# Performance work log

Hardware: AMD Instinct MI355X
Metric: run time of the kernel (lower is better)

Reference implementation:

```python
import jax, jax.numpy as jnp
import numpy as np

NHLOG2PI = -0.5 * np.log(2.0 * np.pi)


def _log_bessel_i(nu, x):
    # log I_nu(x) via the uniform asymptotic expansion (A&S 9.7.7), accurate for large nu.
    # Replaces the original mpmath besseli loop with a device-friendly closed form.
    z = x / nu
    sq = jnp.sqrt(1.0 + z * z)
    eta = sq + jnp.log(z) - jnp.log1p(sq)
    t = 1.0 / sq
    u1 = (3.0 * t - 5.0 * t ** 3) / 24.0  # first correction term
    return nu * eta - 0.5 * jnp.log(2.0 * jnp.pi * nu) - 0.25 * jnp.log1p(z * z) + jnp.log1p(u1 / nu)


def _log_vmf_partition(d, kappa):
    # log C_d(kappa) = d*(-0.5 log 2pi) + s*log(kappa) - log I_s(kappa), s = d/2 - 1
    s = 0.5 * d - 1.0
    return d * NHLOG2PI + s * jnp.log(kappa) - _log_bessel_i(s, kappa)


def reference(id_samples, kappa_weight, prototypes, targets, project_dim):
    eps_n = 1e-12  # torch F.normalize eps
    eps_c = 1e-8   # torch cosine_similarity eps
    # --- sequential normalized EMA scatter-update of prototypes (faithful to per-sample loop) ---
    norm_samples = id_samples / jnp.maximum(
        jnp.linalg.norm(id_samples, axis=-1, keepdims=True), eps_n)

    def step(protos, inp):
        s_n, t = inp
        new = 0.05 * s_n + 0.95 * protos[t]
        new = new / jnp.maximum(jnp.linalg.norm(new), eps_n)
        return protos.at[t].set(new), None

    protos, _ = jax.lax.scan(step, prototypes, (norm_samples, targets))
    protos = jax.lax.stop_gradient(protos)  # original uses .data.detach()

    # --- cosine similarity [N, C] without materializing the repeated tensors ---
    x_n = id_samples / jnp.maximum(jnp.linalg.norm(id_samples, axis=-1, keepdims=True), eps_c)
    p_n = protos / jnp.maximum(jnp.linalg.norm(protos, axis=-1, keepdims=True), eps_c)
    cos = x_n @ p_n.T  # [N, C]

    kap = jax.nn.relu(kappa_weight)  # [C]
    logits = cos * kap[None, :]
    weight_before_exp = jnp.exp(_log_vmf_partition(float(project_dim), kap))[None, :]  # [1, C]

    # --- weighted vMF NLL ---
    num = weight_before_exp * jnp.exp(logits)
    pred = num / num.sum(-1, keepdims=True)
    p_t = jnp.take_along_axis(pred, targets[:, None], axis=1)[:, 0]
    return -jnp.mean(jnp.log(p_t + 1e-6))


def setup_inputs() -> dict:
    key = jax.random.key(0)
    k1, k2, k3 = jax.random.split(key, 3)
    N, C, D = 16384, 2048, 32
    return {
        "id_samples": jax.random.normal(k1, (N, D), dtype=jnp.float32),
        "kappa_weight": jax.random.uniform(k2, (C,), dtype=jnp.float32),
        "prototypes": jnp.zeros((C, D), dtype=jnp.float32),
        "targets": jax.random.randint(k3, (N,), 0, C),
        "project_dim": D,
    }
```

## Files before the change

kernel.cpp:

```cpp
#include <hip/hip_runtime.h>
#include <hip/hip_bf16.h>
#include <math.h>

#define D 32
#define CAP 28
#define CPB 4
#define SBT 512
#define SSM 16

typedef __attribute__((ext_vector_type(8))) short short8v;
typedef __attribute__((ext_vector_type(4))) float float4v;

static __device__ __forceinline__ unsigned short f2bf(float f) {
    union { __hip_bfloat16 h; unsigned short u; } cv;
    cv.h = __float2bfloat16(f);
    return cv.u;
}
static __device__ __forceinline__ float bf2f(unsigned short u) {
    union { float f; unsigned int i; } c;
    c.i = ((unsigned int)u) << 16;
    return c.f;
}
static __device__ __forceinline__ short8v cvt8(float4 u0, float4 u1) {
    short8v o;
    o[0] = (short)f2bf(u0.x); o[1] = (short)f2bf(u0.y);
    o[2] = (short)f2bf(u0.z); o[3] = (short)f2bf(u0.w);
    o[4] = (short)f2bf(u1.x); o[5] = (short)f2bf(u1.y);
    o[6] = (short)f2bf(u1.z); o[7] = (short)f2bf(u1.w);
    return o;
}

__global__ void k_bucket(const int* __restrict__ tgt, int* __restrict__ cnt,
                         int* __restrict__ list2d, int N) {
    int i = blockIdx.x * blockDim.x + threadIdx.x;
    if (i < N) {
        int t = tgt[i];
        int pos = atomicAdd(&cnt[t], 1);
        if (pos < CAP) list2d[t * CAP + pos] = i;
    }
}

__global__ void __launch_bounds__(64 * CPB)
k_gram(const float* __restrict__ x, const int* __restrict__ tgt,
       const int* __restrict__ cnt, const int* __restrict__ list2d,
       const float* __restrict__ p_in, const float* __restrict__ kw,
       unsigned short* __restrict__ qb, float* __restrict__ w,
       int N, int C, float dval) {
    __shared__ int   slist[CPB][CAP];
    __shared__ float Graw[CPB][32][33];
    __shared__ float invv[CPB][32];
    __shared__ float gamS[CPB][CAP];
    int tid = threadIdx.x, b = blockIdx.x;
    int lane = tid & 63, wv = tid >> 6;
    int c = b * CPB + wv, e = lane & 31;

    int n = cnt[c];
    float kap = fmaxf(kw[c], 0.0f);

    if (n <= CAP) {
        int idx = (lane < n) ? list2d[c * CAP + lane] : 0x7fffffff;
        int rank = 0;
        for (int j = 0; j < n; ++j) { int v = __shfl(idx, j); rank += (v < idx) ? 1 : 0; }
        if (lane < n) slist[wv][rank] = idx;

        int m = lane & 15, kg = lane >> 4, k0 = kg * 8;
        short8v A0 = {0,0,0,0,0,0,0,0}, A1 = {0,0,0,0,0,0,0,0};
        if (m < n) {
            const float4* px = (const float4*)(x + (size_t)slist[wv][m] * D + k0);
            A0 = cvt8(px[0], px[1]);
        }
        {
            int r = 16 + m;
            if (r < n) {
                const float4* px = (const float4*)(x + (size_t)slist[wv][r] * D + k0);
                A1 = cvt8(px[0], px[1]);
            } else if (r == 31) {
                const float4* px = (const float4*)(p_in + (size_t)c * D + k0);
                A1 = cvt8(px[0], px[1]);
            }
        }
        float4v z = {0.f, 0.f, 0.f, 0.f};
        float4v g00 = __builtin_amdgcn_mfma_f32_16x16x32_bf16(A0, A0, z, 0, 0, 0);
        float4v g01 = __builtin_amdgcn_mfma_f32_16x16x32_bf16(A0, A1, z, 0, 0, 0);
        float4v g10 = __builtin_amdgcn_mfma_f32_16x16x32_bf16(A1, A0, z, 0, 0, 0);
        float4v g11 = __builtin_amdgcn_mfma_f32_16x16x32_bf16(A1, A1, z, 0, 0, 0);
#pragma unroll
        for (int r = 0; r < 4; ++r) {
            int rr = kg * 4 + r;
            Graw[wv][rr][m]           = g00[r];
            Graw[wv][rr][16 + m]      = g01[r];
            Graw[wv][16 + rr][m]      = g10[r];
            Graw[wv][16 + rr][16 + m] = g11[r];
        }
        if (lane < 32)
            invv[wv][lane] = 1.0f / fmaxf(sqrtf(Graw[wv][lane][lane]), 1e-12f);

        float B = 1.0f, U2 = Graw[wv][31][31];
        for (int kk = 0; kk < n; ++kk) {
            const float* grow = &Graw[wv][kk][0];
            float a0 = 0.f, a1 = 0.f, a2 = 0.f, a3 = 0.f;
            int j = 0;
            for (; j + 4 <= kk; j += 4) {
                a0 = fmaf(gamS[wv][j],     grow[j],     a0);
                a1 = fmaf(gamS[wv][j + 1], grow[j + 1], a1);
                a2 = fmaf(gamS[wv][j + 2], grow[j + 2], a2);
                a3 = fmaf(gamS[wv][j + 3], grow[j + 3], a3);
            }
            for (; j < kk; ++j) a0 = fmaf(gamS[wv][j], grow[j], a0);
            float dot = grow[31] + ((a0 + a1) + (a2 + a3));
            float dsum = invv[wv][kk] * B * dot;
            float m2 = 0.0025f + fmaf(0.9025f, U2, 0.095f * dsum);
            float mm = fmaxf(sqrtf(m2), 1e-12f);
            B *= 0.95f / mm;
            float gk = (0.05f * invv[wv][kk]) / (mm * B);
            if (lane == 0) gamS[wv][kk] = gk;
            U2 = 1.0f;
        }

        float coef0 = (m < n) ? gamS[wv][m] : 0.0f;
        float coef1 = (16 + m < n) ? gamS[wv][16 + m] : ((16 + m == 31) ? 1.0f : 0.0f);
        float part[8];
#pragma unroll
        for (int jj = 0; jj < 8; ++jj)
            part[jj] = fmaf(coef0, bf2f((unsigned short)A0[jj]),
                            coef1 * bf2f((unsigned short)A1[jj]));
#pragma unroll
        for (int off = 1; off < 16; off <<= 1) {
#pragma unroll
            for (int jj = 0; jj < 8; ++jj)
                part[jj] += __shfl_xor(part[jj], off);
        }
        float ssl = 0.f;
#pragma unroll
        for (int jj = 0; jj < 8; ++jj) ssl = fmaf(part[jj], part[jj], ssl);
        ssl += __shfl_xor(ssl, 16);
        ssl += __shfl_xor(ssl, 32);
        float pninv = 1.0f / fmaxf(sqrtf(ssl), 1e-8f);
        float sc = kap * pninv;
        if (m == 0) {
            short8v ov;
#pragma unroll
            for (int jj = 0; jj < 8; ++jj) ov[jj] = (short)f2bf(sc * part[jj]);
            *(short8v*)(qb + (size_t)c * D + k0) = ov;
        }
    } else {
        float p = p_in[(size_t)c * D + e];
        for (int ii = 0; ii < N; ii += 64) {
            unsigned long long mb = __ballot(tgt[ii + lane] == c);
            while (mb) {
                int j = __ffsll(mb) - 1;
                mb &= (mb - 1);
                float v = x[(size_t)(ii + j) * D + e];
                float s2 = v * v;
                s2 += __shfl_xor(s2, 16); s2 += __shfl_xor(s2, 8); s2 += __shfl_xor(s2, 4);
                s2 += __shfl_xor(s2, 2);  s2 += __shfl_xor(s2, 1);
                float s = v / fmaxf(sqrtf(s2), 1e-12f);
                p = fmaf(0.05f, s, 0.95f * p);
                float pp = p * p;
                pp += __shfl_xor(pp, 16); pp += __shfl_xor(pp, 8); pp += __shfl_xor(pp, 4);
                pp += __shfl_xor(pp, 2);  pp += __shfl_xor(pp, 1);
                p = p / fmaxf(sqrtf(pp), 1e-12f);
            }
        }
        float pp = p * p;
        pp += __shfl_xor(pp, 16); pp += __shfl_xor(pp, 8); pp += __shfl_xor(pp, 4);
        pp += __shfl_xor(pp, 2);  pp += __shfl_xor(pp, 1);
        float pn = p / fmaxf(sqrtf(pp), 1e-8f);
        if (lane < D) qb[(size_t)c * D + e] = f2bf(kap * pn);
    }

    if (lane == 0) {
        float nu = 0.5f * dval - 1.0f;
        float zz = kap / nu, z2 = zz * zz;
        float sq = sqrtf(1.0f + z2);
        float t  = 1.0f / sq;
        float u1 = (3.0f * t - 5.0f * t * t * t) * (1.0f / 24.0f);
        float lw = dval * (-0.918938533204672742f)
                 + nu * (logf(nu) + log1pf(sq) - sq)
                 + 0.5f * logf(6.2831853071795864f * nu)
                 + 0.25f * log1pf(z2)
                 - log1pf(u1 / nu);
        w[c] = __expf(lw);
    }
}

__global__ void __launch_bounds__(SBT)
k_score(const float* __restrict__ x, const int* __restrict__ tgt,
        const unsigned short* __restrict__ qb, const float* __restrict__ w,
        float* __restrict__ part, int N, int C) {
    __shared__ float Sl[8][SSM];
    __shared__ float Lt[SSM];
    int tid = threadIdx.x, b = blockIdx.x;
    int lane = tid & 63, wv = tid >> 6;
    int m = lane & 15, kg = lane >> 4, k0 = kg * 8;
    int s0 = b * SSM;

    short8v a0;
    {
        const float4* px = (const float4*)(x + (size_t)(s0 + m) * D + k0);
        float4 u0 = px[0], u1 = px[1];
        float ss = u0.x*u0.x + u0.y*u0.y + u0.z*u0.z + u0.w*u0.w
                 + u1.x*u1.x + u1.y*u1.y + u1.z*u1.z + u1.w*u1.w;
        ss += __shfl_xor(ss, 16); ss += __shfl_xor(ss, 32);
        float inv = 1.0f / fmaxf(sqrtf(ss), 1e-8f);
        float4 v0, v1;
        v0.x = u0.x*inv; v0.y = u0.y*inv; v0.z = u0.z*inv; v0.w = u0.w*inv;
        v1.x = u1.x*inv; v1.y = u1.y*inv; v1.z = u1.z*inv; v1.w = u1.w*inv;
        a0 = cvt8(v0, v1);
    }

    int tr0[4];
#pragma unroll
    for (int r = 0; r < 4; ++r) tr0[r] = tgt[s0 + kg * 4 + r];

    float4v z = {0.f, 0.f, 0.f, 0.f};
    float4v sa0 = z;
    int ntiles = C >> 7;
    for (int jt = 0; jt < ntiles; ++jt) {
        int c0 = (wv * ntiles + jt) * 16;
        short8v bfrag = *(const short8v*)(qb + (size_t)(c0 + m) * D + k0);
        float wl = w[c0 + m];
        float4v acc0 = __builtin_amdgcn_mfma_f32_16x16x32_bf16(a0, bfrag, z, 0, 0, 0);
#pragma unroll
        for (int r = 0; r < 4; ++r) {
            if (c0 + m == tr0[r]) Lt[kg * 4 + r] = acc0[r];
            sa0[r] = fmaf(wl, __expf(acc0[r]), sa0[r]);
        }
    }
#pragma unroll
    for (int off = 1; off < 16; off <<= 1) {
#pragma unroll
        for (int r = 0; r < 4; ++r) sa0[r] += __shfl_xor(sa0[r], off);
    }
    if (m == 0) {
#pragma unroll
        for (int r = 0; r < 4; ++r) Sl[wv][kg * 4 + r] = sa0[r];
    }
    __syncthreads();

    if (wv == 0) {
        float val = 0.f;
        if (lane < SSM) {
            int s = lane;
            float S = ((Sl[0][s] + Sl[1][s]) + (Sl[2][s] + Sl[3][s]))
                    + ((Sl[4][s] + Sl[5][s]) + (Sl[6][s] + Sl[7][s]));
            int t = tgt[s0 + s];
            val = logf(w[t] * __expf(Lt[s]) / S + 1e-6f);
        }
        val += __shfl_xor(val, 32); val += __shfl_xor(val, 16); val += __shfl_xor(val, 8);
        val += __shfl_xor(val, 4);  val += __shfl_xor(val, 2);  val += __shfl_xor(val, 1);
        if (lane == 0) part[b] = val;
    }
}

__global__ void k_out(const float* __restrict__ part, float* __restrict__ out,
                      int N, int nblk) {
    __shared__ float red[8];
    int tid = threadIdx.x, lane = tid & 63, wv = tid >> 6;
    float v = 0.f;
    if (tid < nblk)       v += part[tid];
    if (tid + 512 < nblk) v += part[tid + 512];
    v += __shfl_xor(v, 32); v += __shfl_xor(v, 16); v += __shfl_xor(v, 8);
    v += __shfl_xor(v, 4);  v += __shfl_xor(v, 2);  v += __shfl_xor(v, 1);
    if (lane == 0) red[wv] = v;
    __syncthreads();
    if (tid == 0)
        out[0] = -(((red[0] + red[1]) + (red[2] + red[3]))
                 + ((red[4] + red[5]) + (red[6] + red[7]))) / (float)N;
}

extern "C" void kernel_launch(void* const* d_in, const int* in_sizes, int n_in,
                              void* d_out, int out_size, void* d_ws, size_t ws_size,
                              hipStream_t stream) {
    const float* x    = (const float*)d_in[0];
    const float* kw   = (const float*)d_in[1];
    const float* p_in = (const float*)d_in[2];
    const int*   tgt  = (const int*)d_in[3];
    int C = in_sizes[1];
    int N = in_sizes[3];
    float dval = (float)(in_sizes[2] / C);
    int nblk = N / SSM;

    int* cnt    = (int*)d_ws;
    int* list2d = cnt + C;
    unsigned short* qb = (unsigned short*)(list2d + (size_t)C * CAP);
    float* w    = (float*)(qb + (size_t)C * D);
    float* part = w + C;
    (void)n_in; (void)out_size; (void)ws_size;

    hipMemsetAsync(cnt, 0, (size_t)C * sizeof(int), stream);
    k_bucket<<<(N + 255) / 256, 256, 0, stream>>>(tgt, cnt, list2d, N);
    k_gram<<<C / CPB, 64 * CPB, 0, stream>>>(x, tgt, cnt, list2d, p_in, kw, qb, w, N, C, dval);
    k_score<<<nblk, SBT, 0, stream>>>(x, tgt, qb, w, part, N, C);
    k_out<<<1, 512, 0, stream>>>(part, (float*)d_out, N, nblk);
}
```

Baseline: 40.75 us.

## Fuse target bucketing into gram kernel with per-block shared-memory scan

New measurement: 41.26 us. About the same (+1.2%).

```diff
diff --git a/kernel.cpp b/kernel.cpp
--- a/kernel.cpp
+++ b/kernel.cpp
@@ -30,22 +30,13 @@
     return o;
 }
 
-__global__ void k_bucket(const int* __restrict__ tgt, int* __restrict__ cnt,
-                         int* __restrict__ list2d, int N) {
-    int i = blockIdx.x * blockDim.x + threadIdx.x;
-    if (i < N) {
-        int t = tgt[i];
-        int pos = atomicAdd(&cnt[t], 1);
-        if (pos < CAP) list2d[t * CAP + pos] = i;
-    }
-}
-
 __global__ void __launch_bounds__(64 * CPB)
 k_gram(const float* __restrict__ x, const int* __restrict__ tgt,
-       const int* __restrict__ cnt, const int* __restrict__ list2d,
        const float* __restrict__ p_in, const float* __restrict__ kw,
        unsigned short* __restrict__ qb, float* __restrict__ w,
        int N, int C, float dval) {
+    __shared__ int   lcnt[CPB];
+    __shared__ int   llist[CPB][CAP];
     __shared__ int   slist[CPB][CAP];
     __shared__ float Graw[CPB][32][33];
     __shared__ float invv[CPB][32];
@@ -54,11 +45,22 @@
     int lane = tid & 63, wv = tid >> 6;
     int c = b * CPB + wv, e = lane & 31;
 
-    int n = cnt[c];
+    if (tid < CPB) lcnt[tid] = 0;
+    __syncthreads();
+    for (int i = tid; i < N; i += 64 * CPB) {
+        int r = tgt[i] - b * CPB;
+        if ((unsigned)r < (unsigned)CPB) {
+            int pos = atomicAdd(&lcnt[r], 1);
+            if (pos < CAP) llist[r][pos] = i;
+        }
+    }
+    __syncthreads();
+
+    int n = lcnt[wv];
     float kap = fmaxf(kw[c], 0.0f);
 
     if (n <= CAP) {
-        int idx = (lane < n) ? list2d[c * CAP + lane] : 0x7fffffff;
+        int idx = (lane < n) ? llist[wv][lane] : 0x7fffffff;
         int rank = 0;
         for (int j = 0; j < n; ++j) { int v = __shfl(idx, j); rank += (v < idx) ? 1 : 0; }
         if (lane < n) slist[wv][rank] = idx;
@@ -281,16 +283,12 @@
     float dval = (float)(in_sizes[2] / C);
     int nblk = N / SSM;
 
-    int* cnt    = (int*)d_ws;
-    int* list2d = cnt + C;
-    unsigned short* qb = (unsigned short*)(list2d + (size_t)C * CAP);
+    unsigned short* qb = (unsigned short*)d_ws;
     float* w    = (float*)(qb + (size_t)C * D);
     float* part = w + C;
     (void)n_in; (void)out_size; (void)ws_size;
 
-    hipMemsetAsync(cnt, 0, (size_t)C * sizeof(int), stream);
-    k_bucket<<<(N + 255) / 256, 256, 0, stream>>>(tgt, cnt, list2d, N);
-    k_gram<<<C / CPB, 64 * CPB, 0, stream>>>(x, tgt, cnt, list2d, p_in, kw, qb, w, N, C, dval);
+    k_gram<<<C / CPB, 64 * CPB, 0, stream>>>(x, tgt, p_in, kw, qb, w, N, C, dval);
     k_score<<<nblk, SBT, 0, stream>>>(x, tgt, qb, w, part, N, C);
     k_out<<<1, 512, 0, stream>>>(part, (float*)d_out, N, nblk);
 }
```
